# Performance work log

Hardware: AMD Instinct MI355X
Metric: run time of the kernel (lower is better)

The kernel has to match this reference:

```python
import jax, jax.numpy as jnp
import numpy as np

NUM_HEADS = 8
LN_EPS = 1e-5


def setup_inputs() -> dict:
    key = jax.random.key(0)
    k1, k2, k3 = jax.random.split(key, 3)
    B, N, C = 1, 4096, 256
    before = jax.random.normal(k1, (B, N, C), dtype=jnp.float32)
    after = jax.random.normal(k2, (B, N, C), dtype=jnp.float32)
    W_qkv = jax.random.normal(k3, (3 * C, C), dtype=jnp.float32) * (C ** -0.5)
    d = C // NUM_HEADS
    gamma = jnp.ones((d,), dtype=jnp.float32)
    beta = jnp.zeros((d,), dtype=jnp.float32)
    return {"before": before, "after": after, "W_qkv": W_qkv, "gamma": gamma, "beta": beta}


def _qkv_norm(x, W_qkv, gamma, beta, H):
    # x: [B,N,C] -> q,k,v each [B,H,N,d], LayerNorm over d applied to all of qkv
    B, N, C = x.shape
    d = C // H
    t = jnp.einsum('bnc,oc->bno', x, W_qkv)            # [B,N,3C]
    t = t.reshape(B, N, 3, H, d).transpose(2, 0, 3, 1, 4)  # [3,B,H,N,d]
    mu = jnp.mean(t, axis=-1, keepdims=True)
    var = jnp.mean(jnp.square(t - mu), axis=-1, keepdims=True)
    t = (t - mu) * jax.lax.rsqrt(var + LN_EPS) * gamma + beta
    return t[0], t[1], t[2]


def _cross_attn(q, k, v, scale):
    # q,k,v: [B,H,N,d] -> context [B,N,C]
    attn = jax.nn.softmax(jnp.einsum('bhqd,bhkd->bhqk', q, k) * scale, axis=-1)
    ctx = jnp.einsum('bhqk,bhkd->bhqd', attn, v)
    B, H, N, d = ctx.shape
    return ctx.transpose(0, 2, 1, 3).reshape(B, N, H * d)


def reference(before, after, W_qkv, gamma, beta):
    H = NUM_HEADS
    C = before.shape[-1]
    d = C // H
    scale = d ** -0.5
    q_b, k_b, v_b = _qkv_norm(before, W_qkv, gamma, beta, H)
    q_a, k_a, v_a = _qkv_norm(after, W_qkv, gamma, beta, H)
    context_a = _cross_attn(q_b, k_a, v_a, scale)  # before attends to after
    context_b = _cross_attn(q_a, k_b, v_b, scale)  # after attends to before
    return (context_b, context_a)
```

## Files before the change

kernel.cpp:

```cpp
#include <hip/hip_runtime.h>


typedef __attribute__((ext_vector_type(8))) short short8;
typedef __attribute__((ext_vector_type(4))) float float4v;
typedef __attribute__((ext_vector_type(4))) unsigned int uint4v;

#define NTOK 4096
#define CDIM 256
#define HEADS 8
#define DHEAD 32

#define QOFF 0
#define KOFF (2*HEADS*NTOK*DHEAD)
#define VOFF (2*(2*HEADS*NTOK*DHEAD))
#define WOFF (3*(2*HEADS*NTOK*DHEAD))

__device__ inline unsigned short f2bf(float f) {
    union { float f; unsigned u; } v; v.f = f;
    unsigned r = v.u + 0x7FFFu + ((v.u >> 16) & 1u);
    return (unsigned short)(r >> 16);
}

__global__ __launch_bounds__(256) void wconv_kernel(
    const float* __restrict__ W, unsigned short* __restrict__ ws)
{
    int idx = blockIdx.x*256 + threadIdx.x;
    int R = idx >> 5, oct = idx & 31;
    int C = oct * 8;
    const float4* p = reinterpret_cast<const float4*>(W + R*CDIM + C);
    float4 a = p[0], b = p[1];
    short8 f;
    f[0]=(short)f2bf(a.x); f[1]=(short)f2bf(a.y); f[2]=(short)f2bf(a.z); f[3]=(short)f2bf(a.w);
    f[4]=(short)f2bf(b.x); f[5]=(short)f2bf(b.y); f[6]=(short)f2bf(b.z); f[7]=(short)f2bf(b.w);
    int o32 = R >> 5, r = R & 31;
    int kk = C >> 5, quad = (C >> 3) & 3;
    int dst = o32*8192 + (kk*2 + (r>>4))*512 + (quad*16 + (r&15))*8;
    *reinterpret_cast<short8*>(ws + WOFF + dst) = f;
}

__global__ __launch_bounds__(256) void qkv_ln_kernel(
    const float* __restrict__ before, const float* __restrict__ after,
    const float* __restrict__ gamma, const float* __restrict__ beta,
    unsigned short* __restrict__ ws)
{
    const int tid  = threadIdx.x;
    const int lane = tid & 63;
    const int w    = tid >> 6;
    const int quad = lane >> 4;
    const int l16  = lane & 15;
    const int rt   = blockIdx.x >> 3;
    const int oq   = blockIdx.x & 7;

    const int mrow_frag = rt*64 + w*16 + l16;
    const int inp_f = mrow_frag >> 12;
    const int n_f   = mrow_frag & 4095;
    const float* x = inp_f ? after : before;

    short8 afrag[8];
#pragma unroll
    for (int kk = 0; kk < 8; kk++) {
        const float4* p = reinterpret_cast<const float4*>(x + n_f*CDIM + kk*32 + quad*8);
        float4 a = p[0], b = p[1];
        short8 f;
        f[0]=(short)f2bf(a.x); f[1]=(short)f2bf(a.y); f[2]=(short)f2bf(a.z); f[3]=(short)f2bf(a.w);
        f[4]=(short)f2bf(b.x); f[5]=(short)f2bf(b.y); f[6]=(short)f2bf(b.z); f[7]=(short)f2bf(b.w);
        afrag[kk] = f;
    }

    const float g0  = gamma[l16], g1  = gamma[16+l16];
    const float be0 = beta[l16],  be1 = beta[16+l16];
    const float cscale = 0.17677669529663687f * 1.4426950408889634f;

    const int mrow_out  = rt*64 + w*16 + quad*4;
    const int inp_o     = mrow_out >> 12;
    const int n_o_base  = mrow_out & 4095;

    const unsigned short* wbf = ws + WOFF;

    for (int o32 = oq*3; o32 < oq*3 + 3; o32++) {
        const unsigned short* wb = wbf + o32*8192 + lane*8;
        float4v acc0 = {0.f,0.f,0.f,0.f}, acc1 = {0.f,0.f,0.f,0.f};
#pragma unroll
        for (int kk = 0; kk < 8; kk++) {
            short8 b0 = *reinterpret_cast<const short8*>(wb + (kk*2    )*512);
            short8 b1 = *reinterpret_cast<const short8*>(wb + (kk*2 + 1)*512);
            acc0 = __builtin_amdgcn_mfma_f32_16x16x32_bf16(afrag[kk], b0, acc0, 0,0,0);
            acc1 = __builtin_amdgcn_mfma_f32_16x16x32_bf16(afrag[kk], b1, acc1, 0,0,0);
        }

        const int which = o32 >> 3;
        const int h     = o32 & 7;
        unsigned short* qk = ws + (which == 0 ? QOFF : KOFF) + ((inp_o*HEADS + h)*NTOK)*DHEAD;
        unsigned short* vb = ws + VOFF + ((inp_o*HEADS + h)*128)*1024;
        const float qs = (which == 0) ? cscale : 1.0f;

#pragma unroll
        for (int i = 0; i < 4; i++) {
            float sum = acc0[i] + acc1[i];
            float sq  = acc0[i]*acc0[i] + acc1[i]*acc1[i];
#pragma unroll
            for (int m = 1; m < 16; m <<= 1) {
                sum += __shfl_xor(sum, m);
                sq  += __shfl_xor(sq,  m);
            }
            float mu   = sum * (1.0f/32.0f);
            float var  = sq * (1.0f/32.0f) - mu*mu;
            float rstd = rsqrtf(var + 1e-5f);
            float v0 = ((acc0[i]-mu)*rstd*g0 + be0) * qs;
            float v1 = ((acc1[i]-mu)*rstd*g1 + be1) * qs;
            int n = n_o_base + i;
            if (which < 2) {
                qk[n*DHEAD + l16]      = f2bf(v0);
                qk[n*DHEAD + 16 + l16] = f2bf(v1);
            } else {
                int kb = n >> 5, ki = n & 31;
                int slot = ((ki & 15) >> 2)*8 + (ki & 3) + ((ki >> 4) << 2);
                int off  = ((slot >> 3)*16 + l16)*8 + (slot & 7);
                vb[kb*1024 + off]       = f2bf(v0);
                vb[kb*1024 + 512 + off] = f2bf(v1);
            }
        }
    }
}

__global__ __launch_bounds__(256, 4) void attn_kernel(
    const unsigned short* __restrict__ ws, float* __restrict__ out)
{
    __shared__ float comb[2][32][34];

    const int b    = blockIdx.x;
    const int xcd  = b & 7;
    const int i_   = b >> 3;
    const int combo = xcd*2 + (i_ >> 6);
    const int h  = combo & 7;
    const int X  = combo >> 3;
    const int qb = i_ & 63;

    const int qinp = 1 - X, kvinp = X;
    const int tid  = threadIdx.x;
    const int lane = tid & 63;
    const int w    = tid >> 6;
    const int qh   = w & 1;
    const int kh   = w >> 1;
    const int quad = lane >> 4;
    const int l16  = lane & 15;

    const unsigned short* qbase = ws + QOFF + ((qinp*HEADS + h)*NTOK)*DHEAD;
    const unsigned short* kbase = ws + KOFF + ((kvinp*HEADS + h)*NTOK)*DHEAD;
    const unsigned short* vbase = ws + VOFF + ((kvinp*HEADS + h)*128)*1024;

    const int q0 = qb*64 + qh*32;
    const short8 qf0 = *reinterpret_cast<const short8*>(qbase + (q0 + l16)*DHEAD      + quad*8);
    const short8 qf1 = *reinterpret_cast<const short8*>(qbase + (q0 + 16 + l16)*DHEAD + quad*8);

    const unsigned short* kp = kbase + (kh*2048 + l16)*DHEAD + quad*8;
    const unsigned short* vp = vbase + (kh*64)*1024 + lane*8;

    const short8 ones = {0x3F80,0x3F80,0x3F80,0x3F80,0x3F80,0x3F80,0x3F80,0x3F80};

    float4v O00 = {0,0,0,0}, O01 = {0,0,0,0}, O10 = {0,0,0,0}, O11 = {0,0,0,0};
    float4v L0  = {0,0,0,0}, L1  = {0,0,0,0};

    for (int j = 0; j < 16; j++) {
#pragma unroll
        for (int grp = 0; grp < 4; grp++) {
            const int ko = j*128 + grp*32;
            const int kb = j*4 + grp;
            short8 kf0 = *reinterpret_cast<const short8*>(kp + (ko     )*DHEAD);
            short8 kf1 = *reinterpret_cast<const short8*>(kp + (ko + 16)*DHEAD);
            short8 v0  = *reinterpret_cast<const short8*>(vp + kb*1024);
            short8 v1  = *reinterpret_cast<const short8*>(vp + kb*1024 + 512);
#pragma unroll
            for (int s = 0; s < 2; s++) {
                const short8 qf = s ? qf1 : qf0;
                float4v z = {0,0,0,0};
                float4v S0 = __builtin_amdgcn_mfma_f32_16x16x32_bf16(kf0, qf, z, 0,0,0);
                float4v S1 = __builtin_amdgcn_mfma_f32_16x16x32_bf16(kf1, qf, z, 0,0,0);
                union { float f; unsigned u; } u0,u1,u2,u3,u4,u5,u6,u7;
                u0.f = __builtin_amdgcn_exp2f(S0[0]);
                u1.f = __builtin_amdgcn_exp2f(S0[1]);
                u2.f = __builtin_amdgcn_exp2f(S0[2]);
                u3.f = __builtin_amdgcn_exp2f(S0[3]);
                u4.f = __builtin_amdgcn_exp2f(S1[0]);
                u5.f = __builtin_amdgcn_exp2f(S1[1]);
                u6.f = __builtin_amdgcn_exp2f(S1[2]);
                u7.f = __builtin_amdgcn_exp2f(S1[3]);
                union { short8 s8; uint4v u4v; } pfr;
                pfr.u4v[0] = __builtin_amdgcn_perm(u1.u, u0.u, 0x07060302u);
                pfr.u4v[1] = __builtin_amdgcn_perm(u3.u, u2.u, 0x07060302u);
                pfr.u4v[2] = __builtin_amdgcn_perm(u5.u, u4.u, 0x07060302u);
                pfr.u4v[3] = __builtin_amdgcn_perm(u7.u, u6.u, 0x07060302u);
                if (s == 0) {
                    O00 = __builtin_amdgcn_mfma_f32_16x16x32_bf16(pfr.s8, v0,   O00, 0,0,0);
                    O01 = __builtin_amdgcn_mfma_f32_16x16x32_bf16(pfr.s8, v1,   O01, 0,0,0);
                    L0  = __builtin_amdgcn_mfma_f32_16x16x32_bf16(pfr.s8, ones, L0,  0,0,0);
                } else {
                    O10 = __builtin_amdgcn_mfma_f32_16x16x32_bf16(pfr.s8, v0,   O10, 0,0,0);
                    O11 = __builtin_amdgcn_mfma_f32_16x16x32_bf16(pfr.s8, v1,   O11, 0,0,0);
                    L1  = __builtin_amdgcn_mfma_f32_16x16x32_bf16(pfr.s8, ones, L1,  0,0,0);
                }
            }
        }
    }

    if (kh == 1) {
#pragma unroll
        for (int s = 0; s < 2; s++)
#pragma unroll
            for (int i = 0; i < 4; i++) {
                int row = s*16 + quad*4 + i;
                comb[qh][row][l16]      = (s ? O10[i] : O00[i]);
                comb[qh][row][16 + l16] = (s ? O11[i] : O01[i]);
                if (l16 == 0) comb[qh][row][32] = (s ? L1[i] : L0[i]);
            }
    }
    __syncthreads();

    if (kh == 0) {
        float* ob = out + (size_t)X*NTOK*CDIM + h*DHEAD;
#pragma unroll
        for (int s = 0; s < 2; s++) {
#pragma unroll
            for (int i = 0; i < 4; i++) {
                int row = s*16 + quad*4 + i;
                float l = (s ? L1[i] : L0[i]) + comb[qh][row][32];
                float inv = 1.0f / l;
                float a = ((s ? O10[i] : O00[i]) + comb[qh][row][l16])      * inv;
                float bb = ((s ? O11[i] : O01[i]) + comb[qh][row][16 + l16]) * inv;
                int orow = q0 + row;
                ob[orow*CDIM + l16]      = a;
                ob[orow*CDIM + 16 + l16] = bb;
            }
        }
    }
}

extern "C" void kernel_launch(void* const* d_in, const int* in_sizes, int n_in,
                              void* d_out, int out_size, void* d_ws, size_t ws_size,
                              hipStream_t stream)
{
    const float* before = (const float*)d_in[0];
    const float* after  = (const float*)d_in[1];
    const float* W      = (const float*)d_in[2];
    const float* gamma  = (const float*)d_in[3];
    const float* beta   = (const float*)d_in[4];
    float* out          = (float*)d_out;
    unsigned short* ws  = (unsigned short*)d_ws;

    hipLaunchKernelGGL(wconv_kernel, dim3(96), dim3(256), 0, stream, W, ws);
    hipLaunchKernelGGL(qkv_ln_kernel, dim3(1024), dim3(256), 0, stream,
                       before, after, gamma, beta, ws);
    hipLaunchKernelGGL(attn_kernel, dim3(1024), dim3(256), 0, stream, ws, out);
}
```

Baseline: 140.2 us.

## Split keys four ways per block, each wave handling all 64 queries

```diff
diff --git a/kernel.cpp b/kernel.cpp
--- a/kernel.cpp
+++ b/kernel.cpp
@@ -19,6 +19,24 @@
     union { float f; unsigned u; } v; v.f = f;
     unsigned r = v.u + 0x7FFFu + ((v.u >> 16) & 1u);
     return (unsigned short)(r >> 16);
+}
+
+__device__ inline short8 exp_pack(float4v S0, float4v S1) {
+    union { float f; unsigned u; } u0,u1,u2,u3,u4,u5,u6,u7;
+    u0.f = __builtin_amdgcn_exp2f(S0[0]);
+    u1.f = __builtin_amdgcn_exp2f(S0[1]);
+    u2.f = __builtin_amdgcn_exp2f(S0[2]);
+    u3.f = __builtin_amdgcn_exp2f(S0[3]);
+    u4.f = __builtin_amdgcn_exp2f(S1[0]);
+    u5.f = __builtin_amdgcn_exp2f(S1[1]);
+    u6.f = __builtin_amdgcn_exp2f(S1[2]);
+    u7.f = __builtin_amdgcn_exp2f(S1[3]);
+    union { short8 s8; uint4v u4v; } p;
+    p.u4v[0] = __builtin_amdgcn_perm(u1.u, u0.u, 0x07060302u);
+    p.u4v[1] = __builtin_amdgcn_perm(u3.u, u2.u, 0x07060302u);
+    p.u4v[2] = __builtin_amdgcn_perm(u5.u, u4.u, 0x07060302u);
+    p.u4v[3] = __builtin_amdgcn_perm(u7.u, u6.u, 0x07060302u);
+    return p.s8;
 }
 
 __global__ __launch_bounds__(256) void wconv_kernel(
@@ -126,7 +144,7 @@
 __global__ __launch_bounds__(256, 4) void attn_kernel(
     const unsigned short* __restrict__ ws, float* __restrict__ out)
 {
-    __shared__ float comb[2][32][34];
+    __shared__ float comb[3][64][33];
 
     const int b    = blockIdx.x;
     const int xcd  = b & 7;
@@ -140,8 +158,6 @@
     const int tid  = threadIdx.x;
     const int lane = tid & 63;
     const int w    = tid >> 6;
-    const int qh   = w & 1;
-    const int kh   = w >> 1;
     const int quad = lane >> 4;
     const int l16  = lane & 15;
 
@@ -149,87 +165,69 @@
     const unsigned short* kbase = ws + KOFF + ((kvinp*HEADS + h)*NTOK)*DHEAD;
     const unsigned short* vbase = ws + VOFF + ((kvinp*HEADS + h)*128)*1024;
 
-    const int q0 = qb*64 + qh*32;
-    const short8 qf0 = *reinterpret_cast<const short8*>(qbase + (q0 + l16)*DHEAD      + quad*8);
-    const short8 qf1 = *reinterpret_cast<const short8*>(qbase + (q0 + 16 + l16)*DHEAD + quad*8);
-
-    const unsigned short* kp = kbase + (kh*2048 + l16)*DHEAD + quad*8;
-    const unsigned short* vp = vbase + (kh*64)*1024 + lane*8;
+    const int q0 = qb*64;
+    short8 qf[4];
+#pragma unroll
+    for (int qi = 0; qi < 4; qi++)
+        qf[qi] = *reinterpret_cast<const short8*>(qbase + (q0 + qi*16 + l16)*DHEAD + quad*8);
+
+    const unsigned short* kp = kbase + (w*1024 + l16)*DHEAD + quad*8;
+    const unsigned short* vp = vbase + (w*32)*1024 + lane*8;
 
     const short8 ones = {0x3F80,0x3F80,0x3F80,0x3F80,0x3F80,0x3F80,0x3F80,0x3F80};
 
-    float4v O00 = {0,0,0,0}, O01 = {0,0,0,0}, O10 = {0,0,0,0}, O11 = {0,0,0,0};
-    float4v L0  = {0,0,0,0}, L1  = {0,0,0,0};
-
-    for (int j = 0; j < 16; j++) {
-#pragma unroll
-        for (int grp = 0; grp < 4; grp++) {
-            const int ko = j*128 + grp*32;
-            const int kb = j*4 + grp;
-            short8 kf0 = *reinterpret_cast<const short8*>(kp + (ko     )*DHEAD);
-            short8 kf1 = *reinterpret_cast<const short8*>(kp + (ko + 16)*DHEAD);
-            short8 v0  = *reinterpret_cast<const short8*>(vp + kb*1024);
-            short8 v1  = *reinterpret_cast<const short8*>(vp + kb*1024 + 512);
-#pragma unroll
-            for (int s = 0; s < 2; s++) {
-                const short8 qf = s ? qf1 : qf0;
-                float4v z = {0,0,0,0};
-                float4v S0 = __builtin_amdgcn_mfma_f32_16x16x32_bf16(kf0, qf, z, 0,0,0);
-                float4v S1 = __builtin_amdgcn_mfma_f32_16x16x32_bf16(kf1, qf, z, 0,0,0);
-                union { float f; unsigned u; } u0,u1,u2,u3,u4,u5,u6,u7;
-                u0.f = __builtin_amdgcn_exp2f(S0[0]);
-                u1.f = __builtin_amdgcn_exp2f(S0[1]);
-                u2.f = __builtin_amdgcn_exp2f(S0[2]);
-                u3.f = __builtin_amdgcn_exp2f(S0[3]);
-                u4.f = __builtin_amdgcn_exp2f(S1[0]);
-                u5.f = __builtin_amdgcn_exp2f(S1[1]);
-                u6.f = __builtin_amdgcn_exp2f(S1[2]);
-                u7.f = __builtin_amdgcn_exp2f(S1[3]);
-                union { short8 s8; uint4v u4v; } pfr;
-                pfr.u4v[0] = __builtin_amdgcn_perm(u1.u, u0.u, 0x07060302u);
-                pfr.u4v[1] = __builtin_amdgcn_perm(u3.u, u2.u, 0x07060302u);
-                pfr.u4v[2] = __builtin_amdgcn_perm(u5.u, u4.u, 0x07060302u);
-                pfr.u4v[3] = __builtin_amdgcn_perm(u7.u, u6.u, 0x07060302u);
-                if (s == 0) {
-                    O00 = __builtin_amdgcn_mfma_f32_16x16x32_bf16(pfr.s8, v0,   O00, 0,0,0);
-                    O01 = __builtin_amdgcn_mfma_f32_16x16x32_bf16(pfr.s8, v1,   O01, 0,0,0);
-                    L0  = __builtin_amdgcn_mfma_f32_16x16x32_bf16(pfr.s8, ones, L0,  0,0,0);
-                } else {
-                    O10 = __builtin_amdgcn_mfma_f32_16x16x32_bf16(pfr.s8, v0,   O10, 0,0,0);
-                    O11 = __builtin_amdgcn_mfma_f32_16x16x32_bf16(pfr.s8, v1,   O11, 0,0,0);
-                    L1  = __builtin_amdgcn_mfma_f32_16x16x32_bf16(pfr.s8, ones, L1,  0,0,0);
-                }
-            }
-        }
-    }
-
-    if (kh == 1) {
-#pragma unroll
-        for (int s = 0; s < 2; s++)
+    float4v O[4][2], L[4];
+#pragma unroll
+    for (int qi = 0; qi < 4; qi++) {
+        O[qi][0] = (float4v){0,0,0,0};
+        O[qi][1] = (float4v){0,0,0,0};
+        L[qi]    = (float4v){0,0,0,0};
+    }
+    const float4v z = {0,0,0,0};
+
+    for (int t = 0; t < 32; t++) {
+        short8 kf0 = *reinterpret_cast<const short8*>(kp + (t*32     )*DHEAD);
+        short8 kf1 = *reinterpret_cast<const short8*>(kp + (t*32 + 16)*DHEAD);
+        short8 v0  = *reinterpret_cast<const short8*>(vp + t*1024);
+        short8 v1  = *reinterpret_cast<const short8*>(vp + t*1024 + 512);
+#pragma unroll
+        for (int qi = 0; qi < 4; qi++) {
+            float4v S0 = __builtin_amdgcn_mfma_f32_16x16x32_bf16(kf0, qf[qi], z, 0,0,0);
+            float4v S1 = __builtin_amdgcn_mfma_f32_16x16x32_bf16(kf1, qf[qi], z, 0,0,0);
+            short8 pf = exp_pack(S0, S1);
+            O[qi][0] = __builtin_amdgcn_mfma_f32_16x16x32_bf16(pf, v0,   O[qi][0], 0,0,0);
+            O[qi][1] = __builtin_amdgcn_mfma_f32_16x16x32_bf16(pf, v1,   O[qi][1], 0,0,0);
+            L[qi]    = __builtin_amdgcn_mfma_f32_16x16x32_bf16(pf, ones, L[qi],    0,0,0);
+        }
+    }
+
+    if (w > 0) {
+#pragma unroll
+        for (int qi = 0; qi < 4; qi++)
 #pragma unroll
             for (int i = 0; i < 4; i++) {
-                int row = s*16 + quad*4 + i;
-                comb[qh][row][l16]      = (s ? O10[i] : O00[i]);
-                comb[qh][row][16 + l16] = (s ? O11[i] : O01[i]);
-                if (l16 == 0) comb[qh][row][32] = (s ? L1[i] : L0[i]);
+                int row = qi*16 + quad*4 + i;
+                comb[w-1][row][l16]      = O[qi][0][i];
+                comb[w-1][row][16 + l16] = O[qi][1][i];
+                if (l16 == 0) comb[w-1][row][32] = L[qi][i];
             }
     }
     __syncthreads();
 
-    if (kh == 0) {
+    if (w == 0) {
         float* ob = out + (size_t)X*NTOK*CDIM + h*DHEAD;
 #pragma unroll
-        for (int s = 0; s < 2; s++) {
+        for (int qi = 0; qi < 4; qi++) {
 #pragma unroll
             for (int i = 0; i < 4; i++) {
-                int row = s*16 + quad*4 + i;
-                float l = (s ? L1[i] : L0[i]) + comb[qh][row][32];
+                int row = qi*16 + quad*4 + i;
+                float l  = L[qi][i]    + comb[0][row][32]      + comb[1][row][32]      + comb[2][row][32];
+                float a  = O[qi][0][i] + comb[0][row][l16]     + comb[1][row][l16]     + comb[2][row][l16];
+                float bb = O[qi][1][i] + comb[0][row][16+l16]  + comb[1][row][16+l16]  + comb[2][row][16+l16];
                 float inv = 1.0f / l;
-                float a = ((s ? O10[i] : O00[i]) + comb[qh][row][l16])      * inv;
-                float bb = ((s ? O11[i] : O01[i]) + comb[qh][row][16 + l16]) * inv;
                 int orow = q0 + row;
-                ob[orow*CDIM + l16]      = a;
-                ob[orow*CDIM + 16 + l16] = bb;
+                ob[orow*CDIM + l16]      = a  * inv;
+                ob[orow*CDIM + 16 + l16] = bb * inv;
             }
         }
     }
```

After: 137.6 us. About the same (-1.9%).
